# Kernel tuning notes

Hardware: AMD Instinct MI355X
Metric: run time of the kernel (lower is better)

## Reference

```python
import math
import jax, jax.numpy as jnp
import numpy as np

EPS = 1e-5
DIM_E = 448
DIM_H = 64
TOTAL = DIM_E + DIM_H  # 512
C = 1.0


def _project(x, c, margin=1e-3):
    sqrt_c = jnp.sqrt(c)
    norm = jnp.maximum(jnp.linalg.norm(x, axis=-1, keepdims=True), EPS)
    scale = jnp.minimum(((1.0 - margin) / sqrt_c) / norm, 1.0)
    return x * scale


def _mobius_add(x, y, c):
    x2 = jnp.sum(x * x, axis=-1, keepdims=True)
    y2 = jnp.sum(y * y, axis=-1, keepdims=True)
    xy = jnp.sum(x * y, axis=-1, keepdims=True)
    num = (1.0 + 2.0 * c * xy + c * y2) * x + (1.0 - c * x2) * y
    den = jnp.maximum(1.0 + 2.0 * c * xy + c * c * x2 * y2, EPS)
    return _project(num / den, c)


def _exp0(v, c):
    sqrt_c = jnp.sqrt(c)
    norm = jnp.maximum(jnp.linalg.norm(v, axis=-1, keepdims=True), EPS)
    return _project(jnp.tanh(sqrt_c * norm) * v / (sqrt_c * norm), c)


def _dist(x, y, c):
    # x, y broadcast to [B,S,S,dim_h]; returns [B,S,S]
    sqrt_c = jnp.sqrt(c)
    diff = _mobius_add(-x, y, c)
    norm = jnp.minimum(jnp.linalg.norm(diff, axis=-1), (1.0 - 1e-5) / sqrt_c)
    return (2.0 / sqrt_c) * jnp.arctanh(jnp.minimum(sqrt_c * norm, 1.0 - 1e-5))


def setup_inputs() -> dict:
    key = jax.random.key(0)
    ks = jax.random.split(key, 10)
    B, S = 1, 1024
    s = 1.0 / math.sqrt(TOTAL)
    inp = {
        "x": jax.random.normal(ks[0], (B, S, TOTAL), jnp.float32),
        "wq": jax.random.uniform(ks[1], (TOTAL, TOTAL), jnp.float32, -s, s),
        "bq": jax.random.uniform(ks[2], (TOTAL,), jnp.float32, -s, s),
        "wk": jax.random.uniform(ks[3], (TOTAL, TOTAL), jnp.float32, -s, s),
        "bk": jax.random.uniform(ks[4], (TOTAL,), jnp.float32, -s, s),
        "wv": jax.random.uniform(ks[5], (TOTAL, TOTAL), jnp.float32, -s, s),
        "bv": jax.random.uniform(ks[6], (TOTAL,), jnp.float32, -s, s),
        "wo": jax.random.uniform(ks[7], (TOTAL, TOTAL), jnp.float32, -s, s),
        "bo": jax.random.uniform(ks[8], (TOTAL,), jnp.float32, -s, s),
        "alpha_unconstrained": jnp.float32(0.0),
    }
    return inp


def reference(x, wq, bq, wk, bk, wv, bv, wo, bo, alpha_unconstrained):
    q = x @ wq.T + bq
    k = x @ wk.T + bk
    v = x @ wv.T + bv
    qe, qh = q[..., :DIM_E], q[..., DIM_E:]
    ke, kh = k[..., :DIM_E], k[..., DIM_E:]
    # Euclidean squared distance [B,S,S] via GEMM expansion
    qn = jnp.sum(qe * qe, axis=-1)  # [B,S]
    kn = jnp.sum(ke * ke, axis=-1)  # [B,S]
    d_e = qn[:, :, None] + kn[:, None, :] - 2.0 * jnp.einsum("bsd,btd->bst", qe, ke)
    # Hyperbolic distance on Poincare ball
    qh_h = _exp0(qh, C)
    kh_h = _exp0(kh, C)
    d_h = _dist(qh_h[:, :, None, :], kh_h[:, None, :, :], C)  # [B,S,S]
    alpha = jax.nn.softplus(alpha_unconstrained)
    dist = d_e + alpha * d_h * d_h
    logits = jnp.clip(-dist / math.sqrt(float(TOTAL)), -50.0, 0.0)
    attn = jax.nn.softmax(logits, axis=-1)
    out = jnp.einsum("bst,btd->bsd", attn, v)
    return out @ wo.T + bo
```

## Files before the change

kernel.cpp:

```cpp
#include <hip/hip_runtime.h>

#define S_LEN 1024
#define D_TOT 512
#define D_E   448

typedef short bf16x8 __attribute__((ext_vector_type(8)));
typedef float f32x4  __attribute__((ext_vector_type(4)));
typedef unsigned short u16;

__device__ __forceinline__ float frcp(float x) {
  float r; asm("v_rcp_f32 %0, %1" : "=v"(r) : "v"(x)); return r;
}

__device__ __forceinline__ float wave_sum64(float v) {
#pragma unroll
  for (int o = 32; o > 0; o >>= 1) v += __shfl_xor(v, o);
  return v;
}

__device__ __forceinline__ u16 bf16rne(float f) {
  unsigned u = __builtin_bit_cast(unsigned, f);
  return (u16)((u + 0x7fffu + ((u >> 16) & 1u)) >> 16);
}

__device__ __forceinline__ void bsplit(float f, u16 &h, u16 &l) {
  unsigned u  = __builtin_bit_cast(unsigned, f);
  unsigned ur = u + 0x7fffu + ((u >> 16) & 1u);
  h = (u16)(ur >> 16);
  float fh = __builtin_bit_cast(float, ur & 0xffff0000u);
  float r  = f - fh;
  l = bf16rne(r);
}

__device__ __forceinline__ void bsplit8(float4 a, float4 b, uint4 &h, uint4 &l) {
  u16 h0,h1,h2,h3,h4,h5,h6,h7, l0,l1,l2,l3,l4,l5,l6,l7;
  bsplit(a.x,h0,l0); bsplit(a.y,h1,l1); bsplit(a.z,h2,l2); bsplit(a.w,h3,l3);
  bsplit(b.x,h4,l4); bsplit(b.y,h5,l5); bsplit(b.z,h6,l6); bsplit(b.w,h7,l7);
  h.x = (unsigned)h0 | ((unsigned)h1<<16); h.y = (unsigned)h2 | ((unsigned)h3<<16);
  h.z = (unsigned)h4 | ((unsigned)h5<<16); h.w = (unsigned)h6 | ((unsigned)h7<<16);
  l.x = (unsigned)l0 | ((unsigned)l1<<16); l.y = (unsigned)l2 | ((unsigned)l3<<16);
  l.z = (unsigned)l4 | ((unsigned)l5<<16); l.w = (unsigned)l6 | ((unsigned)l7<<16);
}

__device__ __forceinline__ uint4 rne8(float4 a, float4 b) {
  uint4 h;
  h.x = (unsigned)bf16rne(a.x) | ((unsigned)bf16rne(a.y)<<16);
  h.y = (unsigned)bf16rne(a.z) | ((unsigned)bf16rne(a.w)<<16);
  h.z = (unsigned)bf16rne(b.x) | ((unsigned)bf16rne(b.y)<<16);
  h.w = (unsigned)bf16rne(b.z) | ((unsigned)bf16rne(b.w)<<16);
  return h;
}

#define MFMA2(ACC)                                                                              \
  _Pragma("unroll") for (int i_ = 0; i_ < 2; ++i_)                                              \
  _Pragma("unroll") for (int j_ = 0; j_ < 2; ++j_) {                                            \
    ACC[i_][j_] = __builtin_amdgcn_mfma_f32_16x16x32_bf16(fAh[i_], fBh[j_], ACC[i_][j_],0,0,0); \
    ACC[i_][j_] = __builtin_amdgcn_mfma_f32_16x16x32_bf16(fAh[i_], fBl[j_], ACC[i_][j_],0,0,0); \
  }

__global__ __launch_bounds__(512,4) void qkv_mfma(
    const float* __restrict__ x,
    const float* __restrict__ wq, const float* __restrict__ bq,
    const float* __restrict__ wk, const float* __restrict__ bk,
    const float* __restrict__ wv, const float* __restrict__ bv,
    u16* __restrict__ Qch,
    u16* __restrict__ Kch, u16* __restrict__ Kcl,
    u16* __restrict__ vTh, u16* __restrict__ vTl,
    float* __restrict__ qnpart, float* __restrict__ knpart,
    float* __restrict__ uh2a, float* __restrict__ vh2a)
{
  __shared__ __align__(16) u16 stage[2][15360];
  float* fbuf = (float*)stage;
  const int z = blockIdx.z;
  const float* W; const float* bias;
  if (z == 0)      { W = wq; bias = bq; }
  else if (z == 1) { W = wk; bias = bk; }
  else             { W = wv; bias = bv; }
  const int mBase = blockIdx.y << 6, nBase = blockIdx.x << 6;
  const int t = threadIdx.x, lane = t & 63, wave = t >> 6;
  const int kg = t >> 8, sub = t & 255;
  const int srow = sub >> 2, scol = (sub & 3) << 3;
  const int kgw = wave >> 2, wr = (wave >> 1) & 1, wc = wave & 1;

  const float* Ag = x + (size_t)(mBase + srow) * D_TOT + scol + kg * 256;
  const float* Bg = W + (size_t)(nBase + srow) * D_TOT + scol + kg * 256;

  const int sb = kg * 7680 + srow * 40 + scol;
  const int fa = kgw * 7680 + (wr * 32 + (lane & 15)) * 40 + ((lane >> 4) << 3);
  const int fb = kgw * 7680 + 2560 + (wc * 32 + (lane & 15)) * 40 + ((lane >> 4) << 3);

  float4 a0 = *(const float4*)Ag, a1 = *(const float4*)(Ag + 4);
  float4 b0 = *(const float4*)Bg, b1 = *(const float4*)(Bg + 4);
  {
    uint4 hB,lB; bsplit8(b0,b1,hB,lB);
    *(uint4*)&stage[0][sb       ] = rne8(a0,a1);
    *(uint4*)&stage[0][sb + 2560] = hB;
    *(uint4*)&stage[0][sb + 5120] = lB;
  }
  a0 = *(const float4*)(Ag + 32); a1 = *(const float4*)(Ag + 36);
  b0 = *(const float4*)(Bg + 32); b1 = *(const float4*)(Bg + 36);

  f32x4 zero = {0.f,0.f,0.f,0.f};
  f32x4 acc[2][2] = {{zero,zero},{zero,zero}};
#pragma unroll
  for (int r = 0; r < 8; ++r) {
    __syncthreads();
    const u16* bufr = stage[r & 1];
    bf16x8 fAh[2], fBh[2], fBl[2];
#pragma unroll
    for (int i = 0; i < 2; ++i) {
      fAh[i] = *(const bf16x8*)&bufr[fa        + i*640];
      fBh[i] = *(const bf16x8*)&bufr[fb        + i*640];
      fBl[i] = *(const bf16x8*)&bufr[fb + 2560 + i*640];
    }
    if (r + 1 < 8) {
      u16* bufw = stage[(r + 1) & 1];
      uint4 hB,lB; bsplit8(b0,b1,hB,lB);
      *(uint4*)&bufw[sb       ] = rne8(a0,a1);
      *(uint4*)&bufw[sb + 2560] = hB;
      *(uint4*)&bufw[sb + 5120] = lB;
      if (r + 2 < 8) {
        const int o = (r + 2) * 32;
        a0 = *(const float4*)(Ag + o); a1 = *(const float4*)(Ag + o + 4);
        b0 = *(const float4*)(Bg + o); b1 = *(const float4*)(Bg + o + 4);
      }
    }
    MFMA2(acc);
  }

  __syncthreads();
  {
    const int r0 = wr*32 + ((lane>>4)<<2);
    const int c0 = wc*32 + (lane&15);
#pragma unroll
    for (int i = 0; i < 2; ++i)
#pragma unroll
      for (int j = 0; j < 2; ++j)
#pragma unroll
        for (int g = 0; g < 4; ++g)
          fbuf[kgw*4352 + (r0 + i*16 + g)*68 + c0 + j*16] = acc[i][j][g];
  }
  __syncthreads();
  const int erow = wave << 3;
  float val[8];
  {
    const float b = bias[nBase + lane];
#pragma unroll
    for (int r = 0; r < 8; ++r)
      val[r] = fbuf[(erow+r)*68 + lane] + fbuf[4352 + (erow+r)*68 + lane] + b;
  }

  if (z == 2) {
    u16 hh[8], ll[8];
#pragma unroll
    for (int r = 0; r < 8; ++r) bsplit(val[r], hh[r], ll[r]);
    const size_t off = (size_t)(nBase + lane) * S_LEN + mBase + erow;
    ushort4 p0{hh[0],hh[1],hh[2],hh[3]}, p1{hh[4],hh[5],hh[6],hh[7]};
    ushort4 q0{ll[0],ll[1],ll[2],ll[3]}, q1{ll[4],ll[5],ll[6],ll[7]};
    *(ushort4*)(vTh + off) = p0; *(ushort4*)(vTh + off + 4) = p1;
    *(ushort4*)(vTl + off) = q0; *(ushort4*)(vTl + off + 4) = q1;
  } else if (z == 1) {
    if (blockIdx.x < 7) {
#pragma unroll
      for (int r = 0; r < 8; ++r) {
        const int s = mBase + erow + r;
        u16 h,l; bsplit(val[r],h,l);
        Kch[(size_t)s*D_TOT + nBase + lane] = h;
        Kcl[(size_t)s*D_TOT + nBase + lane] = l;
        float p = wave_sum64(val[r]*val[r]);
        if (lane == 0) knpart[s*8 + blockIdx.x] = p;
      }
    } else {
#pragma unroll
      for (int r = 0; r < 8; ++r) {
        const int s = mBase + erow + r;
        float n2 = wave_sum64(val[r]*val[r]);
        float nn = sqrtf(n2);
        float n  = fmaxf(nn, 1e-5f);
        float e2n = __expf(2.f*n);
        float th  = 1.f - 2.f*frcp(e2n + 1.f);
        float rn  = frcp(n);
        float pn  = th * nn * rn;
        float scale = fminf(0.999f * frcp(fmaxf(pn, 1e-5f)), 1.f);
        float u = th * rn * scale * val[r];
        float un = pn * scale;
        u16 h,l; bsplit(u,h,l);
        Kch[(size_t)s*D_TOT + nBase + lane] = h;
        Kcl[(size_t)s*D_TOT + nBase + lane] = l;
        if (lane == 0) vh2a[s] = un*un;
      }
    }
  } else {
    if (blockIdx.x < 7) {
#pragma unroll
      for (int r = 0; r < 8; ++r) {
        const int s = mBase + erow + r;
        Qch[(size_t)s*D_TOT + nBase + lane] = bf16rne(val[r]);
        float p = wave_sum64(val[r]*val[r]);
        if (lane == 0) qnpart[s*8 + blockIdx.x] = p;
      }
    } else {
#pragma unroll
      for (int r = 0; r < 8; ++r) {
        const int s = mBase + erow + r;
        float n2 = wave_sum64(val[r]*val[r]);
        float nn = sqrtf(n2);
        float n  = fmaxf(nn, 1e-5f);
        float e2n = __expf(2.f*n);
        float th  = 1.f - 2.f*frcp(e2n + 1.f);
        float rn  = frcp(n);
        float pn  = th * nn * rn;
        float scale = fminf(0.999f * frcp(fmaxf(pn, 1e-5f)), 1.f);
        float u = th * rn * scale * val[r];
        float un = pn * scale;
        Qch[(size_t)s*D_TOT + nBase + lane] = bf16rne(u);
        if (lane == 0) uh2a[s] = un*un;
      }
    }
  }
}

__global__ __launch_bounds__(512,4) void score_mfma(
    const u16* __restrict__ Qch,
    const u16* __restrict__ Kch, const u16* __restrict__ Kcl,
    const float* __restrict__ qnpart, const float* __restrict__ knpart,
    const float* __restrict__ uh2a, const float* __restrict__ vh2a,
    const float* __restrict__ alpha_u,
    u16* __restrict__ Eh, float* __restrict__ rowpart)
{
  __shared__ __align__(16) char shm_[69632];
  __shared__ float rowscal[256];
  u16* stg = (u16*)shm_;
  float* fbuf = (float*)shm_;
  const int t = threadIdx.x, lane = t & 63, wave = t >> 6;
  const int mBase = blockIdx.y << 6, nBase = blockIdx.x << 6;
  if (t < 64) {
    float s_ = 0.f;
#pragma unroll
    for (int c = 0; c < 7; ++c) s_ += qnpart[(mBase+t)*8 + c];
    rowscal[t] = s_;
  } else if (t < 128) {
    float s_ = 0.f;
#pragma unroll
    for (int c = 0; c < 7; ++c) s_ += knpart[(nBase+t-64)*8 + c];
    rowscal[t] = s_;
  } else if (t < 192) rowscal[t] = uh2a[mBase + t - 128];
  else if (t < 256)   rowscal[t] = vh2a[nBase + t - 192];

  const int kg = t >> 8, sub = t & 255;
  const int srow = sub >> 2, scol = (sub & 3) << 3;
  const int kgw = wave >> 2, wr = (wave >> 1) & 1, wc = wave & 1;
  const u16* Agh = Qch + (size_t)(mBase+srow)*D_TOT + scol;
  const u16* Bgh = Kch + (size_t)(nBase+srow)*D_TOT + scol;
  const u16* Bgl = Kcl + (size_t)(nBase+srow)*D_TOT + scol;

  const int sb  = kg * 7680 + srow * 40 + scol;
  const int fa  = kgw * 7680 + (wr * 32 + (lane & 15)) * 40 + ((lane >> 4) << 3);
  const int fbh = kgw * 7680 + 2560 + (wc * 32 + (lane & 15)) * 40 + ((lane >> 4) << 3);

  int kb = kg * 224;
  uint4 rAh = *(const uint4*)(Agh + kb);
  uint4 rBh = *(const uint4*)(Bgh + kb), rBl = *(const uint4*)(Bgl + kb);
  *(uint4*)&stg[sb       ] = rAh;
  *(uint4*)&stg[sb + 2560] = rBh;
  *(uint4*)&stg[sb + 5120] = rBl;
  kb = kg * 224 + 32;
  rAh = *(const uint4*)(Agh + kb);
  rBh = *(const uint4*)(Bgh + kb); rBl = *(const uint4*)(Bgl + kb);

  f32x4 zero = {0.f,0.f,0.f,0.f};
  f32x4 accE[2][2] = {{zero,zero},{zero,zero}};
  f32x4 accH[2][2] = {{zero,zero},{zero,zero}};
#pragma unroll
  for (int r = 0; r < 8; ++r) {
    __syncthreads();
    const u16* bufr = stg + (r & 1) * 15360;
    bf16x8 fAh[2], fBh[2], fBl[2];
#pragma unroll
    for (int i = 0; i < 2; ++i) {
      fAh[i] = *(const bf16x8*)&bufr[fa         + i*640];
      fBh[i] = *(const bf16x8*)&bufr[fbh        + i*640];
      fBl[i] = *(const bf16x8*)&bufr[fbh + 2560 + i*640];
    }
    if (r + 1 < 8) {
      u16* bufw = stg + ((r + 1) & 1) * 15360;
      *(uint4*)&bufw[sb       ] = rAh;
      *(uint4*)&bufw[sb + 2560] = rBh;
      *(uint4*)&bufw[sb + 5120] = rBl;
      if (r + 2 < 8) {
        const int o = (r + 2 < 7) ? (kg*224 + (r+2)*32) : (448 + kg*32);
        rAh = *(const uint4*)(Agh + o);
        rBh = *(const uint4*)(Bgh + o); rBl = *(const uint4*)(Bgl + o);
      }
    }
    if (r < 7) { MFMA2(accE) } else { MFMA2(accH) }
  }

  __syncthreads();
  {
    const int r0 = wr*32 + ((lane>>4)<<2);
    const int c0 = wc*32 + (lane&15);
#pragma unroll
    for (int i = 0; i < 2; ++i)
#pragma unroll
      for (int j = 0; j < 2; ++j)
#pragma unroll
        for (int g = 0; g < 4; ++g) {
          fbuf[       kgw*4352 + (r0 + i*16 + g)*68 + c0 + j*16] = accE[i][j][g];
          fbuf[8704 + kgw*4352 + (r0 + i*16 + g)*68 + c0 + j*16] = accH[i][j][g];
        }
  }
  __syncthreads();
  const int erow = wave << 3;
  float eE[8], eH[8];
#pragma unroll
  for (int r = 0; r < 8; ++r) {
    eE[r] = fbuf[(erow+r)*68 + lane] + fbuf[4352 + (erow+r)*68 + lane];
    eH[r] = fbuf[8704 + (erow+r)*68 + lane] + fbuf[8704 + 4352 + (erow+r)*68 + lane];
  }

  const float alpha = __logf(1.f + __expf(alpha_u[0]));
  const float inv_s = 0.04419417382415922f;
  const float knl = rowscal[64 + lane], v2 = rowscal[192 + lane];
#pragma unroll
  for (int r = 0; r < 8; ++r) {
    const int s = mBase + erow + r;
    const float qns = rowscal[erow + r], u2 = rowscal[128 + erow + r];
    float de   = qns + knl - 2.f * eE[r];
    float dH   = eH[r];
    float Ac   = 1.f - 2.f*dH + v2;
    float Bc   = 1.f - u2;
    float num2 = Ac*Ac*u2 + Bc*Bc*v2 - 2.f*Ac*Bc*dH;
    float den  = fmaxf(1.f - 2.f*dH + u2*v2, 1e-5f);
    float frac = sqrtf(fmaxf(num2, 0.f)) * frcp(den);
    float nrm  = fminf(frac, 0.999f);
    float dh_  = __logf((1.f + nrm) * frcp(1.f - nrm));
    float dist = de + alpha * dh_ * dh_;
    float lg   = fminf(fmaxf(-dist * inv_s, -50.f), 0.f);
    float e    = __expf(lg);
    Eh[(size_t)s*S_LEN + nBase + lane] = bf16rne(e);
    float rs = wave_sum64(e);
    if (lane == 0) rowpart[s*16 + blockIdx.x] = rs;
  }
}

__global__ __launch_bounds__(512,4) void av_mfma(
    const u16* __restrict__ Eh,
    const u16* __restrict__ vTh, const u16* __restrict__ vTl,
    const float* __restrict__ rowpart,
    u16* __restrict__ out1h)
{
  __shared__ __align__(16) u16 stg[25600];
  __shared__ float rinvl[32];
  float* fbuf = (float*)stg;
  const int t = threadIdx.x, lane = t & 63, wave = t >> 6;
  const int mBase = blockIdx.y << 5, nBase = blockIdx.x << 6;
  if (t < 32) {
    float s_ = 0.f;
#pragma unroll
    for (int c = 0; c < 16; ++c) s_ += rowpart[(mBase+t)*16 + c];
    rinvl[t] = 1.f / s_;
  }
  const int kg = t >> 7, sub = t & 127;
  const int arow = sub >> 2, acol = (sub & 3) << 3;
  const int brow0 = sub >> 2, bcol0 = (sub & 3) << 3;
  const int brow1 = (sub + 128) >> 2, bcol1 = ((sub + 128) & 3) << 3;
  const int kgw = wave >> 1, wc = wave & 1;

  const u16* Ag  = Eh  + (size_t)(mBase+arow)*S_LEN + acol + kg*256;
  const u16* B0h = vTh + (size_t)(nBase+brow0)*S_LEN + bcol0 + kg*256;
  const u16* B0l = vTl + (size_t)(nBase+brow0)*S_LEN + bcol0 + kg*256;
  const u16* B1h = vTh + (size_t)(nBase+brow1)*S_LEN + bcol1 + kg*256;
  const u16* B1l = vTl + (size_t)(nBase+brow1)*S_LEN + bcol1 + kg*256;

  const int sA  = kg*6400 + arow*40 + acol;
  const int sB0 = kg*6400 + 1280 + brow0*40 + bcol0;
  const int sB1 = kg*6400 + 1280 + brow1*40 + bcol1;
  const int fa  = kgw*6400 + (lane&15)*40 + ((lane>>4)<<3);
  const int fbh = kgw*6400 + 1280 + (wc*32 + (lane&15))*40 + ((lane>>4)<<3);

  uint4 rA = *(const uint4*)Ag;
  uint4 rb0h = *(const uint4*)B0h, rb0l = *(const uint4*)B0l;
  uint4 rb1h = *(const uint4*)B1h, rb1l = *(const uint4*)B1l;

  f32x4 zero = {0.f,0.f,0.f,0.f};
  f32x4 acc[2][2] = {{zero,zero},{zero,zero}};
#pragma unroll
  for (int r = 0; r < 8; ++r) {
    __syncthreads();
    *(uint4*)&stg[sA        ] = rA;
    *(uint4*)&stg[sB0       ] = rb0h; *(uint4*)&stg[sB0 + 2560] = rb0l;
    *(uint4*)&stg[sB1       ] = rb1h; *(uint4*)&stg[sB1 + 2560] = rb1l;
    if (r + 1 < 8) {
      const int o = (r + 1) * 32;
      rA = *(const uint4*)(Ag + o);
      rb0h = *(const uint4*)(B0h + o); rb0l = *(const uint4*)(B0l + o);
      rb1h = *(const uint4*)(B1h + o); rb1l = *(const uint4*)(B1l + o);
    }
    __syncthreads();
    bf16x8 fAh[2], fBh[2], fBl[2];
#pragma unroll
    for (int i = 0; i < 2; ++i) {
      fAh[i] = *(const bf16x8*)&stg[fa         + i*640];
      fBh[i] = *(const bf16x8*)&stg[fbh        + i*640];
      fBl[i] = *(const bf16x8*)&stg[fbh + 2560 + i*640];
    }
    MFMA2(acc);
  }

  __syncthreads();
  {
    const int r0 = (lane>>4)<<2;
    const int c0 = wc*32 + (lane&15);
#pragma unroll
    for (int i = 0; i < 2; ++i)
#pragma unroll
      for (int j = 0; j < 2; ++j)
#pragma unroll
        for (int g = 0; g < 4; ++g)
          fbuf[kgw*2176 + (r0 + i*16 + g)*68 + c0 + j*16] = acc[i][j][g];
  }
  __syncthreads();
  const int erow = wave << 2;
#pragma unroll
  for (int r = 0; r < 4; ++r) {
    const int row = erow + r;
    float e = fbuf[row*68 + lane] + fbuf[2176 + row*68 + lane]
            + fbuf[4352 + row*68 + lane] + fbuf[6528 + row*68 + lane];
    float v_ = e * rinvl[row];
    const int s = mBase + row;
    out1h[(size_t)s*D_TOT + nBase + lane] = bf16rne(v_);
  }
}

__global__ __launch_bounds__(512,4) void final_mfma(
    const u16* __restrict__ out1h,
    const float* __restrict__ wo, const float* __restrict__ bo,
    float* __restrict__ out)
{
  __shared__ __align__(16) u16 stg[25600];
  float* fbuf = (float*)stg;
  const int t = threadIdx.x, lane = t & 63, wave = t >> 6;
  const int mBase = blockIdx.y << 5, nBase = blockIdx.x << 6;
  const int kg = t >> 7, sub = t & 127;
  const int arow = sub >> 2, acol = (sub & 3) << 3;
  const int brow0 = sub >> 2, bcol0 = (sub & 3) << 3;
  const int brow1 = (sub + 128) >> 2, bcol1 = ((sub + 128) & 3) << 3;
  const int kgw = wave >> 1, wc = wave & 1;

  const u16* Ag = out1h + (size_t)(mBase+arow)*D_TOT + acol + kg*128;
  const float* B0 = wo + (size_t)(nBase+brow0)*D_TOT + bcol0 + kg*128;
  const float* B1 = wo + (size_t)(nBase+brow1)*D_TOT + bcol1 + kg*128;

  const int sA  = kg*6400 + arow*40 + acol;
  const int sB0 = kg*6400 + 1280 + brow0*40 + bcol0;
  const int sB1 = kg*6400 + 1280 + brow1*40 + bcol1;
  const int fa  = kgw*6400 + (lane&15)*40 + ((lane>>4)<<3);
  const int fbh = kgw*6400 + 1280 + (wc*32 + (lane&15))*40 + ((lane>>4)<<3);

  uint4 rA = *(const uint4*)Ag;
  float4 b00 = *(const float4*)B0, b01 = *(const float4*)(B0 + 4);
  float4 b10 = *(const float4*)B1, b11 = *(const float4*)(B1 + 4);

  f32x4 zero = {0.f,0.f,0.f,0.f};
  f32x4 acc[2][2] = {{zero,zero},{zero,zero}};
#pragma unroll
  for (int r = 0; r < 4; ++r) {
    __syncthreads();
    uint4 bh0,bl0,bh1,bl1;
    bsplit8(b00,b01,bh0,bl0); bsplit8(b10,b11,bh1,bl1);
    *(uint4*)&stg[sA        ] = rA;
    *(uint4*)&stg[sB0       ] = bh0; *(uint4*)&stg[sB0 + 2560] = bl0;
    *(uint4*)&stg[sB1       ] = bh1; *(uint4*)&stg[sB1 + 2560] = bl1;
    if (r + 1 < 4) {
      const int o = (r + 1) * 32;
      rA = *(const uint4*)(Ag + o);
      b00 = *(const float4*)(B0 + o); b01 = *(const float4*)(B0 + o + 4);
      b10 = *(const float4*)(B1 + o); b11 = *(const float4*)(B1 + o + 4);
    }
    __syncthreads();
    bf16x8 fAh[2], fBh[2], fBl[2];
#pragma unroll
    for (int i = 0; i < 2; ++i) {
      fAh[i] = *(const bf16x8*)&stg[fa         + i*640];
      fBh[i] = *(const bf16x8*)&stg[fbh        + i*640];
      fBl[i] = *(const bf16x8*)&stg[fbh + 2560 + i*640];
    }
    MFMA2(acc);
  }

  __syncthreads();
  {
    const int r0 = (lane>>4)<<2;
    const int c0 = wc*32 + (lane&15);
#pragma unroll
    for (int i = 0; i < 2; ++i)
#pragma unroll
      for (int j = 0; j < 2; ++j)
#pragma unroll
        for (int g = 0; g < 4; ++g)
          fbuf[kgw*2176 + (r0 + i*16 + g)*68 + c0 + j*16] = acc[i][j][g];
  }
  __syncthreads();
  const int erow = wave << 2;
  const float b = bo[nBase + lane];
#pragma unroll
  for (int r = 0; r < 4; ++r) {
    const int row = erow + r;
    float e = fbuf[row*68 + lane] + fbuf[2176 + row*68 + lane]
            + fbuf[4352 + row*68 + lane] + fbuf[6528 + row*68 + lane];
    out[(size_t)(mBase+row)*D_TOT + nBase + lane] = e + b;
  }
}

extern "C" void kernel_launch(void* const* d_in, const int* in_sizes, int n_in,
                              void* d_out, int out_size, void* d_ws, size_t ws_size,
                              hipStream_t stream)
{
  const float* x   = (const float*)d_in[0];
  const float* wq  = (const float*)d_in[1];
  const float* bq  = (const float*)d_in[2];
  const float* wk  = (const float*)d_in[3];
  const float* bk  = (const float*)d_in[4];
  const float* wv  = (const float*)d_in[5];
  const float* bv  = (const float*)d_in[6];
  const float* wo  = (const float*)d_in[7];
  const float* bo  = (const float*)d_in[8];
  const float* alpha_u = (const float*)d_in[9];
  float* out = (float*)d_out;

  u16* U = (u16*)d_ws;
  u16* Qch   = U + 0;
  u16* Kch   = U + 524288;
  u16* Kcl   = U + 1048576;
  u16* vTh   = U + 1572864;
  u16* vTl   = U + 2097152;
  u16* Eh    = U + 2621440;
  u16* out1h = U + 3670016;
  float* F = (float*)(U + 4194304);
  float* qnpart  = F;
  float* knpart  = F + 8192;
  float* uh2a    = F + 16384;
  float* vh2a    = F + 17408;
  float* rowpart = F + 18432;

  qkv_mfma<<<dim3(8,16,3), 512, 0, stream>>>(x, wq,bq, wk,bk, wv,bv,
      Qch, Kch, Kcl, vTh, vTl, qnpart, knpart, uh2a, vh2a);
  score_mfma<<<dim3(16,16), 512, 0, stream>>>(Qch, Kch, Kcl,
      qnpart, knpart, uh2a, vh2a, alpha_u, Eh, rowpart);
  av_mfma<<<dim3(8,32), 512, 0, stream>>>(Eh, vTh, vTl, rowpart, out1h);
  final_mfma<<<dim3(8,32), 512, 0, stream>>>(out1h, wo, bo, out);
}
```

Before: 42.07 us.

## Drop bf16 hi/lo split for K and V; double-buffer AV staging

Stores K and V as single bf16 values instead of a high/low bf16 pair, halving their memory traffic and the MFMA count in the score and attention-times-V GEMMs. The AV kernel also moves from a single LDS buffer with two barriers per step to a double-buffered pipeline with one barrier per step. The cost is lower precision in the Q·K scores and in the A·V product, which could push results past the tolerance.

After: 38.15 us. 1.1x faster.

```diff
diff --git a/kernel.cpp b/kernel.cpp
--- a/kernel.cpp
+++ b/kernel.cpp
@@ -58,14 +58,17 @@
     ACC[i_][j_] = __builtin_amdgcn_mfma_f32_16x16x32_bf16(fAh[i_], fBl[j_], ACC[i_][j_],0,0,0); \
   }
 
+#define MFMA1(ACC)                                                                              \
+  _Pragma("unroll") for (int i_ = 0; i_ < 2; ++i_)                                              \
+  _Pragma("unroll") for (int j_ = 0; j_ < 2; ++j_)                                              \
+    ACC[i_][j_] = __builtin_amdgcn_mfma_f32_16x16x32_bf16(fAh[i_], fBh[j_], ACC[i_][j_],0,0,0);
+
 __global__ __launch_bounds__(512,4) void qkv_mfma(
     const float* __restrict__ x,
     const float* __restrict__ wq, const float* __restrict__ bq,
     const float* __restrict__ wk, const float* __restrict__ bk,
     const float* __restrict__ wv, const float* __restrict__ bv,
-    u16* __restrict__ Qch,
-    u16* __restrict__ Kch, u16* __restrict__ Kcl,
-    u16* __restrict__ vTh, u16* __restrict__ vTl,
+    u16* __restrict__ Qch, u16* __restrict__ Kch, u16* __restrict__ vTh,
     float* __restrict__ qnpart, float* __restrict__ knpart,
     float* __restrict__ uh2a, float* __restrict__ vh2a)
 {
@@ -151,24 +154,23 @@
   }
 
   if (z == 2) {
-    u16 hh[8], ll[8];
-#pragma unroll
-    for (int r = 0; r < 8; ++r) bsplit(val[r], hh[r], ll[r]);
+    u16 hh[8];
+#pragma unroll
+    for (int r = 0; r < 8; ++r) hh[r] = bf16rne(val[r]);
     const size_t off = (size_t)(nBase + lane) * S_LEN + mBase + erow;
     ushort4 p0{hh[0],hh[1],hh[2],hh[3]}, p1{hh[4],hh[5],hh[6],hh[7]};
-    ushort4 q0{ll[0],ll[1],ll[2],ll[3]}, q1{ll[4],ll[5],ll[6],ll[7]};
     *(ushort4*)(vTh + off) = p0; *(ushort4*)(vTh + off + 4) = p1;
-    *(ushort4*)(vTl + off) = q0; *(ushort4*)(vTl + off + 4) = q1;
-  } else if (z == 1) {
+  } else {
+    u16* Ch = z ? Kch : Qch;
+    float* np_ = z ? knpart : qnpart;
+    float* u2a = z ? vh2a  : uh2a;
     if (blockIdx.x < 7) {
 #pragma unroll
       for (int r = 0; r < 8; ++r) {
         const int s = mBase + erow + r;
-        u16 h,l; bsplit(val[r],h,l);
-        Kch[(size_t)s*D_TOT + nBase + lane] = h;
-        Kcl[(size_t)s*D_TOT + nBase + lane] = l;
+        Ch[(size_t)s*D_TOT + nBase + lane] = bf16rne(val[r]);
         float p = wave_sum64(val[r]*val[r]);
-        if (lane == 0) knpart[s*8 + blockIdx.x] = p;
+        if (lane == 0) np_[s*8 + blockIdx.x] = p;
       }
     } else {
 #pragma unroll
@@ -184,45 +186,15 @@
         float scale = fminf(0.999f * frcp(fmaxf(pn, 1e-5f)), 1.f);
         float u = th * rn * scale * val[r];
         float un = pn * scale;
-        u16 h,l; bsplit(u,h,l);
-        Kch[(size_t)s*D_TOT + nBase + lane] = h;
-        Kcl[(size_t)s*D_TOT + nBase + lane] = l;
-        if (lane == 0) vh2a[s] = un*un;
+        Ch[(size_t)s*D_TOT + nBase + lane] = bf16rne(u);
+        if (lane == 0) u2a[s] = un*un;
       }
     }
-  } else {
-    if (blockIdx.x < 7) {
-#pragma unroll
-      for (int r = 0; r < 8; ++r) {
-        const int s = mBase + erow + r;
-        Qch[(size_t)s*D_TOT + nBase + lane] = bf16rne(val[r]);
-        float p = wave_sum64(val[r]*val[r]);
-        if (lane == 0) qnpart[s*8 + blockIdx.x] = p;
-      }
-    } else {
-#pragma unroll
-      for (int r = 0; r < 8; ++r) {
-        const int s = mBase + erow + r;
-        float n2 = wave_sum64(val[r]*val[r]);
-        float nn = sqrtf(n2);
-        float n  = fmaxf(nn, 1e-5f);
-        float e2n = __expf(2.f*n);
-        float th  = 1.f - 2.f*frcp(e2n + 1.f);
-        float rn  = frcp(n);
-        float pn  = th * nn * rn;
-        float scale = fminf(0.999f * frcp(fmaxf(pn, 1e-5f)), 1.f);
-        float u = th * rn * scale * val[r];
-        float un = pn * scale;
-        Qch[(size_t)s*D_TOT + nBase + lane] = bf16rne(u);
-        if (lane == 0) uh2a[s] = un*un;
-      }
-    }
   }
 }
 
 __global__ __launch_bounds__(512,4) void score_mfma(
-    const u16* __restrict__ Qch,
-    const u16* __restrict__ Kch, const u16* __restrict__ Kcl,
+    const u16* __restrict__ Qch, const u16* __restrict__ Kch,
     const float* __restrict__ qnpart, const float* __restrict__ knpart,
     const float* __restrict__ uh2a, const float* __restrict__ vh2a,
     const float* __restrict__ alpha_u,
@@ -252,21 +224,19 @@
   const int kgw = wave >> 2, wr = (wave >> 1) & 1, wc = wave & 1;
   const u16* Agh = Qch + (size_t)(mBase+srow)*D_TOT + scol;
   const u16* Bgh = Kch + (size_t)(nBase+srow)*D_TOT + scol;
-  const u16* Bgl = Kcl + (size_t)(nBase+srow)*D_TOT + scol;
-
-  const int sb  = kg * 7680 + srow * 40 + scol;
-  const int fa  = kgw * 7680 + (wr * 32 + (lane & 15)) * 40 + ((lane >> 4) << 3);
-  const int fbh = kgw * 7680 + 2560 + (wc * 32 + (lane & 15)) * 40 + ((lane >> 4) << 3);
+
+  const int sb  = kg * 5120 + srow * 40 + scol;
+  const int fa  = kgw * 5120 + (wr * 32 + (lane & 15)) * 40 + ((lane >> 4) << 3);
+  const int fbh = kgw * 5120 + 2560 + (wc * 32 + (lane & 15)) * 40 + ((lane >> 4) << 3);
 
   int kb = kg * 224;
   uint4 rAh = *(const uint4*)(Agh + kb);
-  uint4 rBh = *(const uint4*)(Bgh + kb), rBl = *(const uint4*)(Bgl + kb);
+  uint4 rBh = *(const uint4*)(Bgh + kb);
   *(uint4*)&stg[sb       ] = rAh;
   *(uint4*)&stg[sb + 2560] = rBh;
-  *(uint4*)&stg[sb + 5120] = rBl;
   kb = kg * 224 + 32;
   rAh = *(const uint4*)(Agh + kb);
-  rBh = *(const uint4*)(Bgh + kb); rBl = *(const uint4*)(Bgl + kb);
+  rBh = *(const uint4*)(Bgh + kb);
 
   f32x4 zero = {0.f,0.f,0.f,0.f};
   f32x4 accE[2][2] = {{zero,zero},{zero,zero}};
@@ -274,26 +244,24 @@
 #pragma unroll
   for (int r = 0; r < 8; ++r) {
     __syncthreads();
-    const u16* bufr = stg + (r & 1) * 15360;
-    bf16x8 fAh[2], fBh[2], fBl[2];
+    const u16* bufr = stg + (r & 1) * 10240;
+    bf16x8 fAh[2], fBh[2];
 #pragma unroll
     for (int i = 0; i < 2; ++i) {
-      fAh[i] = *(const bf16x8*)&bufr[fa         + i*640];
-      fBh[i] = *(const bf16x8*)&bufr[fbh        + i*640];
-      fBl[i] = *(const bf16x8*)&bufr[fbh + 2560 + i*640];
+      fAh[i] = *(const bf16x8*)&bufr[fa  + i*640];
+      fBh[i] = *(const bf16x8*)&bufr[fbh + i*640];
     }
     if (r + 1 < 8) {
-      u16* bufw = stg + ((r + 1) & 1) * 15360;
+      u16* bufw = stg + ((r + 1) & 1) * 10240;
       *(uint4*)&bufw[sb       ] = rAh;
       *(uint4*)&bufw[sb + 2560] = rBh;
-      *(uint4*)&bufw[sb + 5120] = rBl;
       if (r + 2 < 8) {
         const int o = (r + 2 < 7) ? (kg*224 + (r+2)*32) : (448 + kg*32);
         rAh = *(const uint4*)(Agh + o);
-        rBh = *(const uint4*)(Bgh + o); rBl = *(const uint4*)(Bgl + o);
+        rBh = *(const uint4*)(Bgh + o);
       }
     }
-    if (r < 7) { MFMA2(accE) } else { MFMA2(accH) }
+    if (r < 7) { MFMA1(accE) } else { MFMA1(accH) }
   }
 
   __syncthreads();
@@ -345,14 +313,13 @@
 }
 
 __global__ __launch_bounds__(512,4) void av_mfma(
-    const u16* __restrict__ Eh,
-    const u16* __restrict__ vTh, const u16* __restrict__ vTl,
+    const u16* __restrict__ Eh, const u16* __restrict__ vTh,
     const float* __restrict__ rowpart,
     u16* __restrict__ out1h)
 {
-  __shared__ __align__(16) u16 stg[25600];
+  __shared__ __align__(16) u16 stage[2][15360];
   __shared__ float rinvl[32];
-  float* fbuf = (float*)stg;
+  float* fbuf = (float*)stage;
   const int t = threadIdx.x, lane = t & 63, wave = t >> 6;
   const int mBase = blockIdx.y << 5, nBase = blockIdx.x << 6;
   if (t < 32) {
@@ -363,49 +330,49 @@
   }
   const int kg = t >> 7, sub = t & 127;
   const int arow = sub >> 2, acol = (sub & 3) << 3;
-  const int brow0 = sub >> 2, bcol0 = (sub & 3) << 3;
-  const int brow1 = (sub + 128) >> 2, bcol1 = ((sub + 128) & 3) << 3;
+  const int brow0 = sub >> 2, brow1 = 32 + (sub >> 2), bcol = (sub & 3) << 3;
   const int kgw = wave >> 1, wc = wave & 1;
 
-  const u16* Ag  = Eh  + (size_t)(mBase+arow)*S_LEN + acol + kg*256;
-  const u16* B0h = vTh + (size_t)(nBase+brow0)*S_LEN + bcol0 + kg*256;
-  const u16* B0l = vTl + (size_t)(nBase+brow0)*S_LEN + bcol0 + kg*256;
-  const u16* B1h = vTh + (size_t)(nBase+brow1)*S_LEN + bcol1 + kg*256;
-  const u16* B1l = vTl + (size_t)(nBase+brow1)*S_LEN + bcol1 + kg*256;
-
-  const int sA  = kg*6400 + arow*40 + acol;
-  const int sB0 = kg*6400 + 1280 + brow0*40 + bcol0;
-  const int sB1 = kg*6400 + 1280 + brow1*40 + bcol1;
-  const int fa  = kgw*6400 + (lane&15)*40 + ((lane>>4)<<3);
-  const int fbh = kgw*6400 + 1280 + (wc*32 + (lane&15))*40 + ((lane>>4)<<3);
+  const u16* Ag = Eh  + (size_t)(mBase+arow)*S_LEN + kg*256 + acol;
+  const u16* B0 = vTh + (size_t)(nBase+brow0)*S_LEN + kg*256 + bcol;
+  const u16* B1 = vTh + (size_t)(nBase+brow1)*S_LEN + kg*256 + bcol;
+
+  const int sA  = kg*3840 + arow*40 + acol;
+  const int sB0 = kg*3840 + 1280 + brow0*40 + bcol;
+  const int sB1 = kg*3840 + 1280 + brow1*40 + bcol;
+  const int fa  = kgw*3840 + (lane&15)*40 + ((lane>>4)<<3);
+  const int fb  = kgw*3840 + 1280 + (wc*32 + (lane&15))*40 + ((lane>>4)<<3);
 
   uint4 rA = *(const uint4*)Ag;
-  uint4 rb0h = *(const uint4*)B0h, rb0l = *(const uint4*)B0l;
-  uint4 rb1h = *(const uint4*)B1h, rb1l = *(const uint4*)B1l;
+  uint4 rb0 = *(const uint4*)B0, rb1 = *(const uint4*)B1;
+  *(uint4*)&stage[0][sA ] = rA;
+  *(uint4*)&stage[0][sB0] = rb0; *(uint4*)&stage[0][sB1] = rb1;
+  rA = *(const uint4*)(Ag + 32);
+  rb0 = *(const uint4*)(B0 + 32); rb1 = *(const uint4*)(B1 + 32);
 
   f32x4 zero = {0.f,0.f,0.f,0.f};
   f32x4 acc[2][2] = {{zero,zero},{zero,zero}};
 #pragma unroll
   for (int r = 0; r < 8; ++r) {
     __syncthreads();
-    *(uint4*)&stg[sA        ] = rA;
-    *(uint4*)&stg[sB0       ] = rb0h; *(uint4*)&stg[sB0 + 2560] = rb0l;
-    *(uint4*)&stg[sB1       ] = rb1h; *(uint4*)&stg[sB1 + 2560] = rb1l;
+    const u16* bufr = stage[r & 1];
+    bf16x8 fAh[2], fBh[2];
+#pragma unroll
+    for (int i = 0; i < 2; ++i) {
+      fAh[i] = *(const bf16x8*)&bufr[fa + i*640];
+      fBh[i] = *(const bf16x8*)&bufr[fb + i*640];
+    }
     if (r + 1 < 8) {
-      const int o = (r + 1) * 32;
-      rA = *(const uint4*)(Ag + o);
-      rb0h = *(const uint4*)(B0h + o); rb0l = *(const uint4*)(B0l + o);
-      rb1h = *(const uint4*)(B1h + o); rb1l = *(const uint4*)(B1l + o);
-    }
-    __syncthreads();
-    bf16x8 fAh[2], fBh[2], fBl[2];
-#pragma unroll
-    for (int i = 0; i < 2; ++i) {
-      fAh[i] = *(const bf16x8*)&stg[fa         + i*640];
-      fBh[i] = *(const bf16x8*)&stg[fbh        + i*640];
-      fBl[i] = *(const bf16x8*)&stg[fbh + 2560 + i*640];
-    }
-    MFMA2(acc);
+      u16* bufw = stage[(r + 1) & 1];
+      *(uint4*)&bufw[sA ] = rA;
+      *(uint4*)&bufw[sB0] = rb0; *(uint4*)&bufw[sB1] = rb1;
+      if (r + 2 < 8) {
+        const int o = (r + 2) * 32;
+        rA = *(const uint4*)(Ag + o);
+        rb0 = *(const uint4*)(B0 + o); rb1 = *(const uint4*)(B1 + o);
+      }
+    }
+    MFMA1(acc);
   }
 
   __syncthreads();
@@ -532,12 +499,10 @@
   u16* U = (u16*)d_ws;
   u16* Qch   = U + 0;
   u16* Kch   = U + 524288;
-  u16* Kcl   = U + 1048576;
-  u16* vTh   = U + 1572864;
-  u16* vTl   = U + 2097152;
-  u16* Eh    = U + 2621440;
-  u16* out1h = U + 3670016;
-  float* F = (float*)(U + 4194304);
+  u16* vTh   = U + 1048576;
+  u16* Eh    = U + 1572864;
+  u16* out1h = U + 2621440;
+  float* F = (float*)(U + 3145728);
   float* qnpart  = F;
   float* knpart  = F + 8192;
   float* uh2a    = F + 16384;
@@ -545,9 +510,9 @@
   float* rowpart = F + 18432;
 
   qkv_mfma<<<dim3(8,16,3), 512, 0, stream>>>(x, wq,bq, wk,bk, wv,bv,
-      Qch, Kch, Kcl, vTh, vTl, qnpart, knpart, uh2a, vh2a);
-  score_mfma<<<dim3(16,16), 512, 0, stream>>>(Qch, Kch, Kcl,
+      Qch, Kch, vTh, qnpart, knpart, uh2a, vh2a);
+  score_mfma<<<dim3(16,16), 512, 0, stream>>>(Qch, Kch,
       qnpart, knpart, uh2a, vh2a, alpha_u, Eh, rowpart);
-  av_mfma<<<dim3(8,32), 512, 0, stream>>>(Eh, vTh, vTl, rowpart, out1h);
+  av_mfma<<<dim3(8,32), 512, 0, stream>>>(Eh, vTh, rowpart, out1h);
   final_mfma<<<dim3(8,32), 512, 0, stream>>>(out1h, wo, bo, out);
 }
```
